# Performance work log

Measured on AMD Instinct MI355X. Metric: run time of the kernel, lower is better.

The kernel has to match this reference:

```python
import jax, jax.numpy as jnp
import numpy as np

TEMP = 0.5  # matches temperature init kwarg
EPS = 1e-12  # F.normalize eps


def _l2norm(x):
    # F.normalize(x, dim=1): x / max(||x||, eps)
    n = jnp.linalg.norm(x, axis=1, keepdims=True)
    return x / jnp.maximum(n, EPS)


def setup_inputs() -> dict:
    key = jax.random.key(0)
    k1, k2 = jax.random.split(key)
    B, D = 4096, 256
    return {
        "x_i": jax.random.normal(k1, (B, D), dtype=jnp.float32),
        "x_j": jax.random.normal(k2, (B, D), dtype=jnp.float32),
    }


def reference(x_i, x_j):
    B = x_i.shape[0]
    z = jnp.concatenate([_l2norm(x_i), _l2norm(x_j)], axis=0)  # [2B, D]
    # cosine similarity of normalized rows == matmul (avoids NxNxD broadcast)
    sim = (z @ z.T) / TEMP  # [2B, 2B]
    idx = jnp.arange(B)
    # diagonals at offsets +B and -B = positive pairs
    pos = jnp.concatenate([sim[idx, idx + B], sim[idx + B, idx]])  # [2B]
    exp_sim = jnp.exp(sim)
    # neg = all off-diagonal entries per row (neg_mask = ~eye(2B))
    exp_neg = exp_sim.sum(axis=1) - jnp.exp(jnp.diagonal(sim))  # [2B]
    exp_pos = jnp.exp(pos)
    loss = -jnp.log(exp_pos / (exp_pos + exp_neg))
    return loss.mean()
```

## Files before the change

### kernel.cpp

```cpp
#include <hip/hip_runtime.h>
#include <hip/hip_bf16.h>

typedef __attribute__((ext_vector_type(8))) int   i32x8;
typedef __attribute__((ext_vector_type(4))) int   i32x4;
typedef __attribute__((ext_vector_type(4))) float f32x4;

constexpr int BB = 4096;
constexpr int D  = 256;
constexpr int R2 = 8192;
constexpr int NSPLIT = 32;
constexpr int CPB = R2 / NSPLIT;
constexpr int NG  = CPB / 16;
constexpr int NTRI = NSPLIT * (NSPLIT + 1) / 2;
constexpr float SCALE = 1.6986436005760381f;
constexpr float E2 = 7.38905609893065f;

__device__ __forceinline__ void async16(const unsigned char* g, unsigned char* l) {
    __builtin_amdgcn_global_load_lds(
        (const __attribute__((address_space(1))) void*)g,
        (__attribute__((address_space(3))) void*)l,
        16, 0, 0);
}

#define MFMA8(A, B, C) \
    __builtin_amdgcn_mfma_scale_f32_16x16x128_f8f6f4((A), (B), (C), 0, 0, 0, 127, 0, 127)

__global__ __launch_bounds__(256) void norm_kernel(const float* __restrict__ xi,
                                                   const float* __restrict__ xj,
                                                   int* __restrict__ z8,
                                                   float* __restrict__ pos,
                                                   float* __restrict__ out) {
    const int wid = threadIdx.x >> 6, lane = threadIdx.x & 63;
    const int k = blockIdx.x * 4 + wid;
    if (blockIdx.x == 0 && threadIdx.x == 0) out[0] = 0.f;
    const float4* a4 = reinterpret_cast<const float4*>(xi + (size_t)k * D);
    const float4* b4 = reinterpret_cast<const float4*>(xj + (size_t)k * D);
    float4 a = a4[lane], b = b4[lane];
    float ssi = a.x*a.x + a.y*a.y + a.z*a.z + a.w*a.w;
    float ssj = b.x*b.x + b.y*b.y + b.z*b.z + b.w*b.w;
    float dot = a.x*b.x + a.y*b.y + a.z*b.z + a.w*b.w;
#pragma unroll
    for (int off = 32; off; off >>= 1) {
        ssi += __shfl_xor(ssi, off);
        ssj += __shfl_xor(ssj, off);
        dot += __shfl_xor(dot, off);
    }
    const float inv_i = 1.0f / fmaxf(sqrtf(ssi), 1e-12f);
    const float inv_j = 1.0f / fmaxf(sqrtf(ssj), 1e-12f);
    const float si = inv_i * SCALE, sj = inv_j * SCALE;
    int pi = __builtin_amdgcn_cvt_pk_fp8_f32(a.x*si, a.y*si, 0, false);
    pi     = __builtin_amdgcn_cvt_pk_fp8_f32(a.z*si, a.w*si, pi, true);
    int pj = __builtin_amdgcn_cvt_pk_fp8_f32(b.x*sj, b.y*sj, 0, false);
    pj     = __builtin_amdgcn_cvt_pk_fp8_f32(b.z*sj, b.w*sj, pj, true);
    z8[(size_t)k * 64 + lane]        = pi;
    z8[(size_t)(k + BB) * 64 + lane] = pj;
    if (lane == 0) pos[k] = dot * inv_i * inv_j * 2.0f;
}

__global__ __launch_bounds__(512, 4) void sim_kernel(const unsigned char* __restrict__ z8,
                                                     float* __restrict__ partial) {
    __shared__ unsigned char tb[CPB * D];
    __shared__ float colws[8][CPB];
    const int tid = threadIdx.x;
    const int wid = tid >> 6, lane = tid & 63;
    const int lrow = lane & 15, quad = lane >> 4;

    int t = blockIdx.x, bx = 0;
    while (t >= (NSPLIT - bx)) { t -= (NSPLIT - bx); ++bx; }
    const int by = bx + t;

    const int r0 = bx * 256 + wid * 32;
    const int cbase = by * CPB;

    {
        const int srcg = (tid & 15) ^ ((tid >> 4) & 15);
        const unsigned char* gs = z8 + (size_t)(cbase + (tid >> 4)) * D + srcg * 16;
        unsigned char* ds = tb + tid * 16;
#pragma unroll
        for (int i = 0; i < 8; ++i)
            async16(gs + (size_t)i * 32 * D, ds + i * 8192);
    }

    const unsigned char* abase = z8 + (size_t)(r0 + lrow) * D + quad * 32;
    i32x8 a0k0 = *reinterpret_cast<const i32x8*>(abase             );
    i32x8 a0k1 = *reinterpret_cast<const i32x8*>(abase        + 128);
    i32x8 a1k0 = *reinterpret_cast<const i32x8*>(abase + 16*D      );
    i32x8 a1k1 = *reinterpret_cast<const i32x8*>(abase + 16*D + 128);
    asm volatile("" : "+v"(a0k0), "+v"(a0k1), "+v"(a1k0), "+v"(a1k1));

    f32x4 racc0 = {0.f,0.f,0.f,0.f}, racc1 = {0.f,0.f,0.f,0.f};

    __syncthreads();

    const int pe0 = (quad * 2) ^ lrow;
    const int pe1 = (8 + quad * 2) ^ lrow;
    const unsigned char* rbp = tb + lrow * D;
#pragma unroll 4
    for (int n = 0; n < NG; ++n) {
        const i32x4 lo0 = *reinterpret_cast<const i32x4*>(rbp + pe0*16);
        const i32x4 hi0 = *reinterpret_cast<const i32x4*>(rbp + (pe0^1)*16);
        const i32x4 lo1 = *reinterpret_cast<const i32x4*>(rbp + pe1*16);
        const i32x4 hi1 = *reinterpret_cast<const i32x4*>(rbp + (pe1^1)*16);
        rbp += 16 * D;
        const i32x8 b0 = __builtin_shufflevector(lo0, hi0, 0,1,2,3,4,5,6,7);
        const i32x8 b1 = __builtin_shufflevector(lo1, hi1, 0,1,2,3,4,5,6,7);

        f32x4 c0 = {0.f,0.f,0.f,0.f}, c1 = {0.f,0.f,0.f,0.f};
        c0 = MFMA8(a0k0, b0, c0);  c0 = MFMA8(a0k1, b1, c0);
        c1 = MFMA8(a1k0, b0, c1);  c1 = MFMA8(a1k1, b1, c1);

        const float e0 = __builtin_amdgcn_exp2f(c0[0]);
        const float e1 = __builtin_amdgcn_exp2f(c0[1]);
        const float e2 = __builtin_amdgcn_exp2f(c0[2]);
        const float e3 = __builtin_amdgcn_exp2f(c0[3]);
        const float e4 = __builtin_amdgcn_exp2f(c1[0]);
        const float e5 = __builtin_amdgcn_exp2f(c1[1]);
        const float e6 = __builtin_amdgcn_exp2f(c1[2]);
        const float e7 = __builtin_amdgcn_exp2f(c1[3]);
        racc0[0] += e0;  racc0[1] += e1;  racc0[2] += e2;  racc0[3] += e3;
        racc1[0] += e4;  racc1[1] += e5;  racc1[2] += e6;  racc1[3] += e7;

        float cs = ((e0 + e1) + (e2 + e3)) + ((e4 + e5) + (e6 + e7));
        cs += __shfl_xor(cs, 16);
        cs += __shfl_xor(cs, 32);
        if (quad == 0) colws[wid][n * 16 + lrow] = cs;
    }

#define REDUCE_STORE(RV, M)                                                     \
    {                                                                           \
        _Pragma("unroll")                                                       \
        for (int j = 0; j < 4; ++j) {                                           \
            float v = (RV)[j];                                                  \
            v += __shfl_xor(v, 1);                                              \
            v += __shfl_xor(v, 2);                                              \
            v += __shfl_xor(v, 4);                                              \
            v += __shfl_xor(v, 8);                                              \
            if (lrow == 0)                                                      \
                partial[(size_t)by * R2 + r0 + (M)*16 + quad*4 + j] = v;        \
        }                                                                       \
    }
    REDUCE_STORE(racc0, 0)
    REDUCE_STORE(racc1, 1)
#undef REDUCE_STORE

    __syncthreads();
    if (bx != by && tid < CPB) {
        float s = 0.f;
#pragma unroll
        for (int w = 0; w < 8; ++w) s += colws[w][tid];
        partial[(size_t)bx * R2 + cbase + tid] = s;
    }
}

__global__ __launch_bounds__(256) void reduce_kernel(const float* __restrict__ partial,
                                                     const float* __restrict__ pos,
                                                     float* __restrict__ out) {
    __shared__ float wsum[4];
    const int tid = threadIdx.x;
    const int r = blockIdx.x * 256 + tid;
    float S = 0.f;
#pragma unroll
    for (int s = 0; s < NSPLIT; ++s) S += partial[(size_t)s * R2 + r];
    const float p = pos[r & (BB - 1)];
    float lsum = __logf(__expf(p) + S - E2) - p;
#pragma unroll
    for (int off = 32; off; off >>= 1) lsum += __shfl_xor(lsum, off);
    if ((tid & 63) == 0) wsum[tid >> 6] = lsum;
    __syncthreads();
    if (tid == 0) {
        float t = wsum[0] + wsum[1] + wsum[2] + wsum[3];
        atomicAdd(out, t * (1.0f / (float)R2));
    }
}

extern "C" void kernel_launch(void* const* d_in, const int* in_sizes, int n_in,
                              void* d_out, int out_size, void* d_ws, size_t ws_size,
                              hipStream_t stream) {
    (void)in_sizes; (void)n_in; (void)out_size; (void)ws_size;
    const float* xi = (const float*)d_in[0];
    const float* xj = (const float*)d_in[1];
    float* out = (float*)d_out;

    unsigned char* z8 = (unsigned char*)d_ws;
    float* partial = (float*)((char*)d_ws + (size_t)R2 * D);
    float* pos     = (float*)((char*)d_ws + (size_t)R2 * D + (size_t)NSPLIT*R2*4);

    norm_kernel<<<BB / 4, 256, 0, stream>>>(xi, xj, (int*)z8, pos, out);
    sim_kernel<<<NTRI, 512, 0, stream>>>(z8, partial);
    reduce_kernel<<<R2 / 256, 256, 0, stream>>>(partial, pos, out);
}
```

Baseline: 84.89 us.

## Split each triangular sim tile into two column halves to double block count

Each triangular tile block is split into two blocks, each handling 128 of the 256 columns. This doubles the grid (528 → 1056 blocks) and halves the LDS tile per block, giving more parallelism and occupancy across the CUs. The partial buffer grows to 64 slots. Column sums are now written as two half-row-block partials, one per 4-warp group, and the reduce kernel sums 64 slots. In exchange, the A fragments are loaded twice and the reduce pass reads twice as much data.

```diff
diff --git a/kernel.cpp b/kernel.cpp
--- a/kernel.cpp
+++ b/kernel.cpp
@@ -9,8 +9,9 @@
 constexpr int D  = 256;
 constexpr int R2 = 8192;
 constexpr int NSPLIT = 32;
-constexpr int CPB = R2 / NSPLIT;
-constexpr int NG  = CPB / 16;
+constexpr int HCOLS  = 128;
+constexpr int NSLOT  = 64;
+constexpr int NGH    = HCOLS / 16;
 constexpr int NTRI = NSPLIT * (NSPLIT + 1) / 2;
 constexpr float SCALE = 1.6986436005760381f;
 constexpr float E2 = 7.38905609893065f;
@@ -59,25 +60,26 @@
 
 __global__ __launch_bounds__(512, 4) void sim_kernel(const unsigned char* __restrict__ z8,
                                                      float* __restrict__ partial) {
-    __shared__ unsigned char tb[CPB * D];
-    __shared__ float colws[8][CPB];
+    __shared__ unsigned char tb[HCOLS * D];
+    __shared__ float colws[8][HCOLS];
     const int tid = threadIdx.x;
     const int wid = tid >> 6, lane = tid & 63;
     const int lrow = lane & 15, quad = lane >> 4;
 
-    int t = blockIdx.x, bx = 0;
+    const int h = blockIdx.x & 1;
+    int t = blockIdx.x >> 1, bx = 0;
     while (t >= (NSPLIT - bx)) { t -= (NSPLIT - bx); ++bx; }
     const int by = bx + t;
 
     const int r0 = bx * 256 + wid * 32;
-    const int cbase = by * CPB;
+    const int cbase = by * 256 + h * HCOLS;
 
     {
         const int srcg = (tid & 15) ^ ((tid >> 4) & 15);
         const unsigned char* gs = z8 + (size_t)(cbase + (tid >> 4)) * D + srcg * 16;
         unsigned char* ds = tb + tid * 16;
 #pragma unroll
-        for (int i = 0; i < 8; ++i)
+        for (int i = 0; i < 4; ++i)
             async16(gs + (size_t)i * 32 * D, ds + i * 8192);
     }
 
@@ -96,7 +98,7 @@
     const int pe1 = (8 + quad * 2) ^ lrow;
     const unsigned char* rbp = tb + lrow * D;
 #pragma unroll 4
-    for (int n = 0; n < NG; ++n) {
+    for (int n = 0; n < NGH; ++n) {
         const i32x4 lo0 = *reinterpret_cast<const i32x4*>(rbp + pe0*16);
         const i32x4 hi0 = *reinterpret_cast<const i32x4*>(rbp + (pe0^1)*16);
         const i32x4 lo1 = *reinterpret_cast<const i32x4*>(rbp + pe1*16);
@@ -136,7 +138,7 @@
             v += __shfl_xor(v, 4);                                              \
             v += __shfl_xor(v, 8);                                              \
             if (lrow == 0)                                                      \
-                partial[(size_t)by * R2 + r0 + (M)*16 + quad*4 + j] = v;        \
+                partial[(size_t)(by*2 + h) * R2 + r0 + (M)*16 + quad*4 + j] = v;\
         }                                                                       \
     }
     REDUCE_STORE(racc0, 0)
@@ -144,11 +146,12 @@
 #undef REDUCE_STORE
 
     __syncthreads();
-    if (bx != by && tid < CPB) {
-        float s = 0.f;
-#pragma unroll
-        for (int w = 0; w < 8; ++w) s += colws[w][tid];
-        partial[(size_t)bx * R2 + cbase + tid] = s;
+    if (bx != by && tid < 2 * HCOLS) {
+        const int c = tid & (HCOLS - 1);
+        const int j = tid >> 7;
+        float s = colws[j*4 + 0][c] + colws[j*4 + 1][c]
+                + colws[j*4 + 2][c] + colws[j*4 + 3][c];
+        partial[(size_t)(bx*2 + j) * R2 + cbase + c] = s;
     }
 }
 
@@ -160,7 +163,7 @@
     const int r = blockIdx.x * 256 + tid;
     float S = 0.f;
 #pragma unroll
-    for (int s = 0; s < NSPLIT; ++s) S += partial[(size_t)s * R2 + r];
+    for (int s = 0; s < NSLOT; ++s) S += partial[(size_t)s * R2 + r];
     const float p = pos[r & (BB - 1)];
     float lsum = __logf(__expf(p) + S - E2) - p;
 #pragma unroll
@@ -183,9 +186,9 @@
 
     unsigned char* z8 = (unsigned char*)d_ws;
     float* partial = (float*)((char*)d_ws + (size_t)R2 * D);
-    float* pos     = (float*)((char*)d_ws + (size_t)R2 * D + (size_t)NSPLIT*R2*4);
+    float* pos     = (float*)((char*)d_ws + (size_t)R2 * D + (size_t)NSLOT*R2*4);
 
     norm_kernel<<<BB / 4, 256, 0, stream>>>(xi, xj, (int*)z8, pos, out);
-    sim_kernel<<<NTRI, 512, 0, stream>>>(z8, partial);
+    sim_kernel<<<NTRI * 2, 512, 0, stream>>>(z8, partial);
     reduce_kernel<<<R2 / 256, 256, 0, stream>>>(partial, pos, out);
 }
```

New measurement: 102.1 us. 1.2x slower.
